# Optimization experiments

Hardware: AMD Instinct MI355X
Metric: run time of the kernel (lower is better)

## Reference

```python
import jax, jax.numpy as jnp
import numpy as np

NUM_HEADS = 16

def _rope(t, cos, sin):
    # t: [B,H,T,hd]; cos/sin: [T,half]
    half = t.shape[-1] // 2
    t1, t2 = t[..., :half], t[..., half:]
    return jnp.concatenate((t1 * cos - t2 * sin, t1 * sin + t2 * cos), axis=-1)

def setup_inputs() -> dict:
    key = jax.random.key(0)
    ks = jax.random.split(key, 5)
    B, T, D = 2, 2048, 2048
    s = 0.02
    return {
        'x': jax.random.normal(ks[0], (B, T, D), jnp.float32),
        'w_qkv': jax.random.normal(ks[1], (3 * D, D), jnp.float32) * s,
        'b_qkv': jax.random.normal(ks[2], (3 * D,), jnp.float32) * s,
        'w_out': jax.random.normal(ks[3], (D, D), jnp.float32) * s,
        'b_out': jax.random.normal(ks[4], (D,), jnp.float32) * s,
    }

def reference(x, w_qkv, b_qkv, w_out, b_out):
    B, T, D = x.shape
    H = NUM_HEADS
    hd = D // H
    half = hd // 2
    # fused QKV projection (torch Linear: x @ W^T + b)
    qkv = (x @ w_qkv.T + b_qkv).reshape(B, T, H, 3, hd)
    q, k, v = qkv[..., 0, :], qkv[..., 1, :], qkv[..., 2, :]
    q, k, v = (jnp.transpose(t, (0, 2, 1, 3)) for t in (q, k, v))  # [B,H,T,hd]
    # RoPE frequencies (buffer computed as in __init__)
    theta = 1.0 / (10000.0 ** (jnp.arange(half, dtype=jnp.float32) / half))
    freq = jnp.arange(T, dtype=jnp.float32)[:, None] * theta[None, :]  # [T,half]
    cos, sin = jnp.cos(freq), jnp.sin(freq)
    q = _rope(q, cos, sin)
    k = _rope(k, cos, sin)
    # causal attention; NOTE: source scales by embed_dim**-0.5
    scale = D ** (-0.5)
    scores = jnp.einsum('bhqd,bhkd->bhqk', q, k) * scale
    mask = jnp.triu(jnp.full((T, T), -1e9, dtype=scores.dtype), k=1)
    weights = jax.nn.softmax(scores + mask, axis=-1)
    attn = jnp.einsum('bhqk,bhkd->bhqd', weights, v)
    attn = jnp.transpose(attn, (0, 2, 1, 3)).reshape(B, T, D)
    return attn @ w_out.T + b_out
```

## Files before the change

kernel.cpp:

```cpp
#include <hip/hip_runtime.h>
#include <math.h>

#define NHEAD 16
#define TSEQ  2048
#define BATCH 2
#define DM    2048

typedef __attribute__((ext_vector_type(8))) short bf16x8;
typedef __attribute__((ext_vector_type(4))) float f32x4;

__device__ __forceinline__ short f2bf(float f) {
    unsigned u = __builtin_bit_cast(unsigned, f);
    u += 0x7fff + ((u >> 16) & 1);
    return (short)(u >> 16);
}
__device__ __forceinline__ float bf2f(short s) {
    unsigned u = ((unsigned)(unsigned short)s) << 16;
    return __builtin_bit_cast(float, u);
}
__device__ __forceinline__ void gload_lds16(const void* g, void* l) {
    __builtin_amdgcn_global_load_lds(
        (const __attribute__((address_space(1))) unsigned int*)g,
        (__attribute__((address_space(3))) unsigned int*)l, 16, 0, 0);
}

__global__ __launch_bounds__(256)
void cast_all(const float* __restrict__ x, short* __restrict__ xb,
              const float* __restrict__ wq, short* __restrict__ wqb,
              const float* __restrict__ wo, short* __restrict__ wob,
              float2* __restrict__ trig)
{
    int bid = blockIdx.x;
    if (bid >= 12288) {
        if (trig) {
            int idx = (bid - 12288) * 256 + threadIdx.x;
            int d = idx >> 11, t = idx & 2047;
            float trev = exp2f(-(float)d * (13.287712379549449f / 64.0f))
                         * 0.15915494309189535f;
            float ang = (float)t * trev;
            float fr = ang - floorf(ang);
            float sn, cs;
            __sincosf(fr * 6.283185307179586f, &sn, &cs);
            trig[idx] = make_float2(cs, sn);
        }
        return;
    }
    const float* src; short* dst; int lb;
    if (bid < 4096)       { src = x;  dst = xb;  lb = bid; }
    else if (bid < 10240) { src = wq; dst = wqb; lb = bid - 4096; }
    else                  { src = wo; dst = wob; lb = bid - 10240; }
    int i = (lb * 256 + threadIdx.x) * 8;
    float4 a = *(const float4*)(src + i);
    float4 b = *(const float4*)(src + i + 4);
    bf16x8 o;
    o[0]=f2bf(a.x); o[1]=f2bf(a.y); o[2]=f2bf(a.z); o[3]=f2bf(a.w);
    o[4]=f2bf(b.x); o[5]=f2bf(b.y); o[6]=f2bf(b.z); o[7]=f2bf(b.w);
    *(bf16x8*)(dst + i) = o;
}

#define BARRIER() __builtin_amdgcn_s_barrier()
#define WAIT_LGKM0() do { asm volatile("s_waitcnt lgkmcnt(0)" ::: "memory"); \
                          __builtin_amdgcn_sched_barrier(0); } while (0)
#define WAIT_VM(N) asm volatile("s_waitcnt vmcnt(" #N ")" ::: "memory")

#define LOAD_A(BUF, MH) do {                                                  \
    const short* base_ = sm + (BUF)*32768 + (MH)*8192;                        \
    _Pragma("unroll")                                                         \
    for (int m_ = 0; m_ < 4; ++m_) {                                          \
        int j_ = wr*64 + m_*16 + lane15;                                      \
        const short* rp_ = base_ + j_*64;                                     \
        int sw_ = (j_ & 7) << 3;                                              \
        af[m_][0] = *(const bf16x8*)(rp_ + ((quad << 3) ^ sw_));              \
        af[m_][1] = *(const bf16x8*)(rp_ + ((32 + (quad << 3)) ^ sw_));       \
    }                                                                         \
} while (0)

#define LOAD_B(BUF, NH, BB) do {                                              \
    const short* base_ = sm + (BUF)*32768 + 16384 + (NH)*8192;                \
    _Pragma("unroll")                                                         \
    for (int n_ = 0; n_ < 2; ++n_) {                                          \
        int j_ = wc*32 + n_*16 + lane15;                                      \
        const short* rp_ = base_ + j_*64;                                     \
        int sw_ = (j_ & 7) << 3;                                              \
        BB[n_][0] = *(const bf16x8*)(rp_ + ((quad << 3) ^ sw_));              \
        BB[n_][1] = *(const bf16x8*)(rp_ + ((32 + (quad << 3)) ^ sw_));       \
    }                                                                         \
} while (0)

#define STAGE_A(T, MH, BUFOFF) do { if ((T) < 32) {                           \
    short* dst_ = sm + (BUFOFF) + ((MH) << 13);                               \
    _Pragma("unroll")                                                         \
    for (int i_ = 0; i_ < 2; ++i_)                                            \
        gload_lds16(pAsrc[i_][MH] + ((T) << 6), dst_ + (i_*512 + tid)*8);     \
    } } while (0)

#define STAGE_B(T, NH, BUFOFF) do { if ((T) < 32) {                           \
    short* dst_ = sm + (BUFOFF) + 16384 + ((NH) << 13);                       \
    _Pragma("unroll")                                                         \
    for (int i_ = 0; i_ < 2; ++i_)                                            \
        gload_lds16(pWsrc[i_][NH] + ((T) << 6), dst_ + (i_*512 + tid)*8);     \
    } } while (0)

#define MMA_Q(MH, NH, BB) do {                                                \
    _Pragma("unroll")                                                         \
    for (int m_ = 0; m_ < 4; ++m_) {                                          \
        _Pragma("unroll")                                                     \
        for (int n_ = 0; n_ < 2; ++n_) {                                      \
            f32x4 c_ = acc[(MH)*4 + m_][(NH)*2 + n_];                         \
            c_ = __builtin_amdgcn_mfma_f32_16x16x32_bf16(af[m_][0], BB[n_][0], c_, 0, 0, 0); \
            c_ = __builtin_amdgcn_mfma_f32_16x16x32_bf16(af[m_][1], BB[n_][1], c_, 0, 0, 0); \
            acc[(MH)*4 + m_][(NH)*2 + n_] = c_;                               \
        }                                                                     \
    }                                                                         \
} while (0)

__global__ __launch_bounds__(512, 2)
void gemm_qkv_rope(const short* __restrict__ A, const short* __restrict__ W,
                   const float* __restrict__ bias, short* __restrict__ qfrag,
                   short* __restrict__ kfrag, short* __restrict__ vfrag,
                   const float2* __restrict__ trig)
{
    __shared__ short sm[65536];
    const int tid = threadIdx.x;
    const int lane = tid & 63, w = tid >> 6;
    const int lane15 = lane & 15, quad = lane >> 4;
    const int wr = w >> 2, wc = w & 3;
    const int row0 = blockIdx.y * 256, col0 = blockIdx.x * 256;

    const short* pAsrc[2][2];
    const short* pWsrc[2][2];
    #pragma unroll
    for (int i_ = 0; i_ < 2; ++i_) {
        int ci = i_*512 + tid, j = ci >> 3, lc = ci & 7;
        int swz = (lc ^ (j & 7)) << 3;
        #pragma unroll
        for (int h = 0; h < 2; ++h) {
            pAsrc[i_][h] = A + (size_t)(row0 + (j & 63) + ((j >> 6) << 7) + h*64) * 2048 + swz;
            pWsrc[i_][h] = W + (size_t)(col0 + (j & 31) + ((j >> 5) << 6) + h*32) * 2048 + swz;
        }
    }

    f32x4 acc[8][4];
    #pragma unroll
    for (int mi = 0; mi < 8; ++mi)
        #pragma unroll
        for (int ni = 0; ni < 4; ++ni)
            acc[mi][ni] = (f32x4){0.f, 0.f, 0.f, 0.f};

    bf16x8 af[4][2], bb0[2][2], bb1[2][2];

    STAGE_A(0, 0, 0);     STAGE_B(0, 0, 0);
    STAGE_A(0, 1, 0);     STAGE_B(0, 1, 0);
    STAGE_A(1, 0, 32768); STAGE_B(1, 0, 32768);
    STAGE_A(1, 1, 32768); STAGE_B(1, 1, 32768);
    WAIT_VM(8);
    BARRIER();

    for (int i = 0; i < 16; ++i) {
        const int ta = 2*i + 2;
        const int tb = 2*i + 3;
        LOAD_A(0, 0);
        LOAD_B(0, 0, bb0);
        BARRIER(); WAIT_LGKM0();
        __builtin_amdgcn_s_setprio(1); MMA_Q(0, 0, bb0); __builtin_amdgcn_s_setprio(0);
        BARRIER();
        LOAD_B(0, 1, bb1);
        STAGE_A(ta, 0, 0); STAGE_B(ta, 0, 0);
        BARRIER(); WAIT_LGKM0();
        __builtin_amdgcn_s_setprio(1); MMA_Q(0, 1, bb1); __builtin_amdgcn_s_setprio(0);
        BARRIER();
        LOAD_A(0, 1);
        STAGE_B(ta, 1, 0);
        BARRIER(); WAIT_LGKM0();
        __builtin_amdgcn_s_setprio(1); MMA_Q(1, 1, bb1); __builtin_amdgcn_s_setprio(0);
        BARRIER();
        STAGE_A(ta, 1, 0);
        if (i == 15) { WAIT_VM(0); } else { WAIT_VM(8); }
        BARRIER();
        __builtin_amdgcn_s_setprio(1); MMA_Q(1, 0, bb0); __builtin_amdgcn_s_setprio(0);
        BARRIER();
        LOAD_A(1, 0);
        LOAD_B(1, 0, bb0);
        BARRIER(); WAIT_LGKM0();
        __builtin_amdgcn_s_setprio(1); MMA_Q(0, 0, bb0); __builtin_amdgcn_s_setprio(0);
        BARRIER();
        LOAD_B(1, 1, bb1);
        STAGE_A(tb, 0, 32768); STAGE_B(tb, 0, 32768);
        BARRIER(); WAIT_LGKM0();
        __builtin_amdgcn_s_setprio(1); MMA_Q(0, 1, bb1); __builtin_amdgcn_s_setprio(0);
        BARRIER();
        LOAD_A(1, 1);
        STAGE_B(tb, 1, 32768);
        BARRIER(); WAIT_LGKM0();
        __builtin_amdgcn_s_setprio(1); MMA_Q(1, 1, bb1); __builtin_amdgcn_s_setprio(0);
        BARRIER();
        STAGE_A(tb, 1, 32768);
        if (i < 15) { WAIT_VM(8); }
        BARRIER();
        __builtin_amdgcn_s_setprio(1); MMA_Q(1, 0, bb0); __builtin_amdgcn_s_setprio(0);
        BARRIER();
    }

    const int b = row0 >> 11;
    const int t0g = row0 & 2047;
    #pragma unroll
    for (int ch = 0; ch < 2; ++ch) {
        const int cidx = (col0 >> 7) + ch;
        const int head = cidx / 3, type = cidx % 3;
        __syncthreads();
        if ((wc >> 1) == ch) {
            #pragma unroll
            for (int ni = 0; ni < 4; ++ni) {
                int d = (wc & 1)*64 + ni*16 + lane15;
                float bv = bias[col0 + ch*128 + d];
                #pragma unroll
                for (int mi = 0; mi < 8; ++mi) {
                    int rowb = wr*128 + mi*16 + quad*4;
                    #pragma unroll
                    for (int r = 0; r < 4; ++r)
                        sm[(rowb + r)*136 + d] = f2bf(acc[mi][ni][r] + bv);
                }
            }
        }
        __syncthreads();
        if (type < 2) {
            const float sc = (type == 0) ? 0.022097086912079608f : 1.0f;
            short* dst = (type == 0 ? qfrag : kfrag) + (size_t)(b*NHEAD + head)*262144;
            #pragma unroll
            for (int it = 0; it < 4; ++it) {
                int c = it*512 + tid;
                int l15 = c & 15, q_ = (c >> 4) & 3, kc = (c >> 6) & 1, rowhi = c >> 7;
                int lrow = rowhi*16 + l15;
                int t = t0g + lrow;
                bf16x8 a8 = *(const bf16x8*)(sm + lrow*136 + kc*32 + q_*8);
                bf16x8 b8 = *(const bf16x8*)(sm + lrow*136 + kc*32 + q_*8 + 64);
                bf16x8 oa, ob;
                if (trig) {
                    const float2* tg = trig + (size_t)(kc*32 + q_*8)*2048 + t;
                    #pragma unroll
                    for (int j = 0; j < 8; ++j) {
                        float2 cs2 = tg[(size_t)j*2048];
                        float va = bf2f(a8[j]), vb = bf2f(b8[j]);
                        oa[j] = f2bf((va*cs2.x - vb*cs2.y)*sc);
                        ob[j] = f2bf((va*cs2.y + vb*cs2.x)*sc);
                    }
                } else {
                    #pragma unroll
                    for (int j = 0; j < 8; ++j) {
                        int d = kc*32 + q_*8 + j;
                        float trev = exp2f(-(float)d * (13.287712379549449f / 64.0f))
                                     * 0.15915494309189535f;
                        float ang = (float)t * trev;
                        float fr = ang - floorf(ang);
                        float sn, cs;
                        __sincosf(fr * 6.283185307179586f, &sn, &cs);
                        float va = bf2f(a8[j]), vb = bf2f(b8[j]);
                        oa[j] = f2bf((va*cs - vb*sn)*sc);
                        ob[j] = f2bf((va*sn + vb*cs)*sc);
                    }
                }
                size_t base = (size_t)((t0g >> 4) + rowhi)*2048 + (q_*16 + l15)*8;
                *(bf16x8*)(dst + base + kc*512)        = oa;
                *(bf16x8*)(dst + base + kc*512 + 1024) = ob;
            }
        } else {
            short* dst = vfrag + (size_t)(b*NHEAD + head)*262144;
            #pragma unroll
            for (int it = 0; it < 8; ++it) {
                int c = it*512 + tid;
                int lane_ = c & 63, rest = c >> 6;
                int q_ = lane_ >> 4, l15 = lane_ & 15;
                int dt = rest & 7, kc2 = (rest >> 3) & 1, kbt = rest >> 4;
                int d = dt*16 + l15;
                bf16x8 v;
                #pragma unroll
                for (int j = 0; j < 8; ++j)
                    v[j] = sm[(kbt*64 + kc2*32 + q_*8 + j)*136 + d];
                *(bf16x8*)(dst + (size_t)((t0g >> 6) + kbt)*8192
                            + dt*1024 + kc2*512 + lane_*8) = v;
            }
        }
    }
}

__global__ __launch_bounds__(256)
void gemm_out(const short* __restrict__ A, const short* __restrict__ W,
              const float* __restrict__ bias, float* __restrict__ Cout,
              int N, int K)
{
    __shared__ short As[128 * 64];
    __shared__ short Bs[128 * 64];
    const int tid = threadIdx.x;
    const int lane = tid & 63, w = tid >> 6;
    const int lane15 = lane & 15, quad = lane >> 4;
    const int wr = w >> 1, wc = w & 1;
    const int row0 = blockIdx.y * 128, col0 = blockIdx.x * 128;

    f32x4 acc[4][4];
    #pragma unroll
    for (int mi = 0; mi < 4; ++mi)
        #pragma unroll
        for (int ni = 0; ni < 4; ++ni)
            acc[mi][ni] = (f32x4){0.f, 0.f, 0.f, 0.f};

    for (int kt = 0; kt < K; kt += 64) {
        __syncthreads();
        #pragma unroll
        for (int i = 0; i < 4; ++i) {
            int ci = i * 256 + tid;
            int row = ci >> 3, lc = ci & 7;
            int gc = lc ^ (row & 7);
            gload_lds16(A + (size_t)(row0 + row) * K + kt + gc * 8, As + ci * 8);
            gload_lds16(W + (size_t)(col0 + row) * K + kt + gc * 8, Bs + ci * 8);
        }
        __syncthreads();
        #pragma unroll
        for (int kc = 0; kc < 2; ++kc) {
            bf16x8 af[4], bfr[4];
            #pragma unroll
            for (int mi = 0; mi < 4; ++mi) {
                int r = wr * 64 + mi * 16 + lane15;
                af[mi] = *(const bf16x8*)(As + r * 64 + ((kc * 4 + quad) ^ (r & 7)) * 8);
            }
            #pragma unroll
            for (int ni = 0; ni < 4; ++ni) {
                int r = wc * 64 + ni * 16 + lane15;
                bfr[ni] = *(const bf16x8*)(Bs + r * 64 + ((kc * 4 + quad) ^ (r & 7)) * 8);
            }
            #pragma unroll
            for (int mi = 0; mi < 4; ++mi)
                #pragma unroll
                for (int ni = 0; ni < 4; ++ni)
                    acc[mi][ni] = __builtin_amdgcn_mfma_f32_16x16x32_bf16(
                        af[mi], bfr[ni], acc[mi][ni], 0, 0, 0);
        }
    }

    #pragma unroll
    for (int mi = 0; mi < 4; ++mi)
        #pragma unroll
        for (int ni = 0; ni < 4; ++ni) {
            int col = col0 + wc * 64 + ni * 16 + lane15;
            float bv = bias[col];
            #pragma unroll
            for (int r = 0; r < 4; ++r) {
                int row = row0 + wr * 64 + mi * 16 + quad * 4 + r;
                Cout[(size_t)row * N + col] = acc[mi][ni][r] + bv;
            }
        }
}

__global__ __launch_bounds__(256)
void attn3(const short* __restrict__ qfrag, const short* __restrict__ kfrag,
           const short* __restrict__ vfrag, short* __restrict__ attnb)
{
    __shared__ short KV[2][16384];
    __shared__ short Pb[4][1152];
    const int tid = threadIdx.x;
    const int lane = tid & 63, w = tid >> 6;
    const int lane15 = lane & 15, quad = lane >> 4;
    const int g = (blockIdx.x + blockIdx.y) & 15;
    const int qb = blockIdx.z ? (15 - g) : g;
    const int h = blockIdx.y, b = blockIdx.z;
    const int bh = b * NHEAD + h;
    const int q0 = qb * 128;
    short* Pw = Pb[w];

    bf16x8 qf[2][4];
    {
        const short* qp = qfrag + (size_t)bh * 262144
                        + (size_t)(qb * 8 + w * 2) * 2048 + lane * 8;
        #pragma unroll
        for (int nq = 0; nq < 2; ++nq)
            #pragma unroll
            for (int kc = 0; kc < 4; ++kc)
                qf[nq][kc] = *(const bf16x8*)(qp + nq * 2048 + kc * 512);
    }

    f32x4 acc[8][2];
    #pragma unroll
    for (int dt = 0; dt < 8; ++dt)
        #pragma unroll
        for (int nq = 0; nq < 2; ++nq)
            acc[dt][nq] = (f32x4){0.f, 0.f, 0.f, 0.f};
    float m_s[2] = {-3e38f, -3e38f}, l_s[2] = {0.f, 0.f};

    const short* kf_src = kfrag + (size_t)bh * 262144;
    const short* vf_src = vfrag + (size_t)bh * 262144;
    const int kb_max = 2 * qb + 1;
    const int qtop = q0 + w * 32 + 31;
    const int diag0 = (q0 + w * 32) >> 6;

    #pragma unroll
    for (int i = 0; i < 4; ++i) {
        int ci = i * 256 + tid;
        gload_lds16(kf_src + ci * 8, KV[0] + ci * 8);
        gload_lds16(vf_src + ci * 8, KV[0] + 8192 + ci * 8);
    }

    for (int kb = 0; kb <= kb_max; ++kb) {
        __syncthreads();
        if (kb < kb_max) {
            const short* ks = kf_src + (size_t)(kb + 1) * 8192;
            const short* vs = vf_src + (size_t)(kb + 1) * 8192;
            short* kd = KV[(kb + 1) & 1];
            #pragma unroll
            for (int i = 0; i < 4; ++i) {
                int ci = i * 256 + tid;
                gload_lds16(ks + ci * 8, kd + ci * 8);
                gload_lds16(vs + ci * 8, kd + 8192 + ci * 8);
            }
        }
        if (kb * 64 > qtop) continue;
        const short* Ks = KV[kb & 1];
        const short* Vs = Ks + 8192;

        f32x4 st[2][4];
        #pragma unroll
        for (int nq = 0; nq < 2; ++nq)
            #pragma unroll
            for (int mi = 0; mi < 4; ++mi)
                st[nq][mi] = (f32x4){0.f, 0.f, 0.f, 0.f};
        #pragma unroll
        for (int mi = 0; mi < 4; ++mi) {
            bf16x8 kf4[4];
            #pragma unroll
            for (int kc = 0; kc < 4; ++kc)
                kf4[kc] = *(const bf16x8*)(Ks + ((mi * 4 + kc) * 64 + lane) * 8);
            #pragma unroll
            for (int kc = 0; kc < 4; ++kc)
                #pragma unroll
                for (int nq = 0; nq < 2; ++nq)
                    st[nq][mi] = __builtin_amdgcn_mfma_f32_16x16x32_bf16(
                        kf4[kc], qf[nq][kc], st[nq][mi], 0, 0, 0);
        }

        if (kb >= diag0) {
            #pragma unroll
            for (int nq = 0; nq < 2; ++nq) {
                int qg = q0 + w * 32 + nq * 16 + lane15;
                #pragma unroll
                for (int mi = 0; mi < 4; ++mi)
                    #pragma unroll
                    for (int r = 0; r < 4; ++r)
                        if (kb * 64 + mi * 16 + quad * 4 + r > qg)
                            st[nq][mi][r] = -3e38f;
            }
        }

        bf16x8 pb[2][2];
        #pragma unroll
        for (int nq = 0; nq < 2; ++nq) {
            float mt = st[nq][0][0];
            #pragma unroll
            for (int mi = 0; mi < 4; ++mi)
                #pragma unroll
                for (int r = 0; r < 4; ++r)
                    mt = fmaxf(mt, st[nq][mi][r]);
            mt = fmaxf(mt, __shfl_xor(mt, 16));
            mt = fmaxf(mt, __shfl_xor(mt, 32));
            float mn = fmaxf(m_s[nq], mt);
            float alpha = __expf(m_s[nq] - mn);
            m_s[nq] = mn;
            float sum = 0.f;
            #pragma unroll
            for (int mi = 0; mi < 4; ++mi)
                #pragma unroll
                for (int r = 0; r < 4; ++r) {
                    float p = __expf(st[nq][mi][r] - mn);
                    st[nq][mi][r] = p;
                    sum += p;
                }
            sum += __shfl_xor(sum, 16);
            sum += __shfl_xor(sum, 32);
            l_s[nq] = l_s[nq] * alpha + sum;
            #pragma unroll
            for (int dt = 0; dt < 8; ++dt) {
                acc[dt][nq][0] *= alpha; acc[dt][nq][1] *= alpha;
                acc[dt][nq][2] *= alpha; acc[dt][nq][3] *= alpha;
            }
            short* pr = Pw + lane15 * 72 + quad * 4;
            #pragma unroll
            for (int mi = 0; mi < 4; ++mi) {
                unsigned lo = (unsigned)(unsigned short)f2bf(st[nq][mi][0])
                            | ((unsigned)(unsigned short)f2bf(st[nq][mi][1]) << 16);
                unsigned hi = (unsigned)(unsigned short)f2bf(st[nq][mi][2])
                            | ((unsigned)(unsigned short)f2bf(st[nq][mi][3]) << 16);
                *(unsigned*)(pr + mi * 16)     = lo;
                *(unsigned*)(pr + mi * 16 + 2) = hi;
            }
            __asm__ volatile("s_waitcnt lgkmcnt(0)" ::: "memory");
            #pragma unroll
            for (int kc2 = 0; kc2 < 2; ++kc2)
                pb[nq][kc2] = *(const bf16x8*)(Pw + lane15 * 72 + kc2 * 32 + quad * 8);
            __asm__ volatile("s_waitcnt lgkmcnt(0)" ::: "memory");
        }

        #pragma unroll
        for (int dt = 0; dt < 8; ++dt)
            #pragma unroll
            for (int kc2 = 0; kc2 < 2; ++kc2) {
                bf16x8 vf = *(const bf16x8*)(Vs + ((dt * 2 + kc2) * 64 + lane) * 8);
                #pragma unroll
                for (int nq = 0; nq < 2; ++nq)
                    acc[dt][nq] = __builtin_amdgcn_mfma_f32_16x16x32_bf16(
                        vf, pb[nq][kc2], acc[dt][nq], 0, 0, 0);
            }
    }

    __syncthreads();
    short* Eb = KV[0];
    #pragma unroll
    for (int nq = 0; nq < 2; ++nq) {
        float inv = 1.f / l_s[nq];
        int qrow = w * 32 + nq * 16 + lane15;
        #pragma unroll
        for (int dt = 0; dt < 8; ++dt) {
            unsigned lo = (unsigned)(unsigned short)f2bf(acc[dt][nq][0] * inv)
                        | ((unsigned)(unsigned short)f2bf(acc[dt][nq][1] * inv) << 16);
            unsigned hi = (unsigned)(unsigned short)f2bf(acc[dt][nq][2] * inv)
                        | ((unsigned)(unsigned short)f2bf(acc[dt][nq][3] * inv) << 16);
            *(unsigned*)(Eb + qrow * 136 + dt * 16 + quad * 4)     = lo;
            *(unsigned*)(Eb + qrow * 136 + dt * 16 + quad * 4 + 2) = hi;
        }
    }
    __syncthreads();
    {
        int r = tid >> 1, half = tid & 1;
        short* orow = attnb + (size_t)(b * TSEQ + q0 + r) * DM + h * 128 + half * 64;
        #pragma unroll
        for (int i = 0; i < 8; ++i)
            *(bf16x8*)(orow + i * 8) =
                *(const bf16x8*)(Eb + r * 136 + half * 64 + i * 8);
    }
}

extern "C" void kernel_launch(void* const* d_in, const int* in_sizes, int n_in,
                              void* d_out, int out_size, void* d_ws, size_t ws_size,
                              hipStream_t stream)
{
    const float* x     = (const float*)d_in[0];
    const float* w_qkv = (const float*)d_in[1];
    const float* b_qkv = (const float*)d_in[2];
    const float* w_out = (const float*)d_in[3];
    const float* b_out = (const float*)d_in[4];
    float* out = (float*)d_out;

    char* ws = (char*)d_ws;
    short* xb    = (short*)(ws);
    short* wqkvb = (short*)(ws + 16777216);
    short* woutb = (short*)(ws + 41943040);
    short* qfrag = (short*)(ws + 50331648);
    short* kfrag = (short*)(ws + 67108864);
    short* vfrag = (short*)(ws + 83886080);
    short* attnb = xb;
    float2* trig = (ws_size >= 100663296ull + 1048576ull)
                 ? (float2*)(ws + 100663296) : nullptr;

    {
        int grid = trig ? 12800 : 12288;
        cast_all<<<grid, 256, 0, stream>>>(x, xb, w_qkv, wqkvb, w_out, woutb, trig);
    }
    {
        dim3 g2(24, 16);
        gemm_qkv_rope<<<g2, 512, 0, stream>>>(xb, wqkvb, b_qkv, qfrag, kfrag, vfrag, trig);
    }
    {
        dim3 g2(16, NHEAD, BATCH);
        attn3<<<g2, 256, 0, stream>>>(qfrag, kfrag, vfrag, attnb);
    }
    {
        dim3 g2(16, 32);
        gemm_out<<<g2, 256, 0, stream>>>(attnb, woutb, b_out, out, 2048, 2048);
    }
}
```

Before: 380.8 us.

## Pipeline output GEMM with triple-buffered LDS and 128x256 tiles

Rewrites the output projection GEMM to use 512 threads per block computing 128x256 tiles. Global-to-LDS loads for two stages ahead go into a three-slot ring buffer, with vmcnt waits and setprio around the MFMA bursts. This overlaps memory loads with matrix math and halves the W reloads per output, at the cost of more LDS (144KB) and only 256 blocks, which risks lower occupancy and tail imbalance.

Result: no change. 388.2 us (+1.9%).

```diff
diff --git a/kernel.cpp b/kernel.cpp
--- a/kernel.cpp
+++ b/kernel.cpp
@@ -283,18 +283,56 @@
     }
 }
 
-__global__ __launch_bounds__(256)
+#define OSTAGE(T) do { if ((T) < 32) {                                        \
+    short* dst_ = smo + ((T) % 3) * 24576;                                    \
+    const int kt_ = (T) << 6;                                                 \
+    _Pragma("unroll")                                                         \
+    for (int i_ = 0; i_ < 2; ++i_) {                                          \
+        int ci_ = i_*512 + tid;                                               \
+        int r_ = ci_ >> 3, lc_ = ci_ & 7;                                     \
+        gload_lds16(A + (size_t)(row0 + r_)*2048 + kt_ + ((lc_ ^ (r_ & 7)) << 3), \
+                    dst_ + ci_*8);                                            \
+    }                                                                         \
+    _Pragma("unroll")                                                         \
+    for (int i_ = 0; i_ < 4; ++i_) {                                          \
+        int ci_ = i_*512 + tid;                                               \
+        int r_ = ci_ >> 3, lc_ = ci_ & 7;                                     \
+        gload_lds16(W + (size_t)(col0 + r_)*2048 + kt_ + ((lc_ ^ (r_ & 7)) << 3), \
+                    dst_ + 8192 + ci_*8);                                     \
+    } } } while (0)
+
+#define OLRD(Ab, Bb, KC) do {                                                 \
+    _Pragma("unroll")                                                         \
+    for (int m_ = 0; m_ < 4; ++m_) {                                          \
+        int r_ = wr*64 + m_*16 + lane15;                                      \
+        af[m_] = *(const bf16x8*)((Ab) + r_*64 + ((((KC)*4 + quad) ^ (r_ & 7)) << 3)); \
+    }                                                                         \
+    _Pragma("unroll")                                                         \
+    for (int n_ = 0; n_ < 4; ++n_) {                                          \
+        int r_ = wc*64 + n_*16 + lane15;                                      \
+        bb[n_] = *(const bf16x8*)((Bb) + r_*64 + ((((KC)*4 + quad) ^ (r_ & 7)) << 3)); \
+    }                                                                         \
+} while (0)
+
+#define OMMA() do {                                                           \
+    _Pragma("unroll")                                                         \
+    for (int m_ = 0; m_ < 4; ++m_)                                            \
+        _Pragma("unroll")                                                     \
+        for (int n_ = 0; n_ < 4; ++n_)                                        \
+            acc[m_][n_] = __builtin_amdgcn_mfma_f32_16x16x32_bf16(            \
+                af[m_], bb[n_], acc[m_][n_], 0, 0, 0);                        \
+} while (0)
+
+__global__ __launch_bounds__(512, 2)
 void gemm_out(const short* __restrict__ A, const short* __restrict__ W,
-              const float* __restrict__ bias, float* __restrict__ Cout,
-              int N, int K)
+              const float* __restrict__ bias, float* __restrict__ Cout)
 {
-    __shared__ short As[128 * 64];
-    __shared__ short Bs[128 * 64];
+    __shared__ short smo[73728];
     const int tid = threadIdx.x;
     const int lane = tid & 63, w = tid >> 6;
     const int lane15 = lane & 15, quad = lane >> 4;
-    const int wr = w >> 1, wc = w & 1;
-    const int row0 = blockIdx.y * 128, col0 = blockIdx.x * 128;
+    const int wr = w >> 2, wc = w & 3;
+    const int row0 = blockIdx.y * 128, col0 = blockIdx.x * 256;
 
     f32x4 acc[4][4];
     #pragma unroll
@@ -303,49 +341,37 @@
         for (int ni = 0; ni < 4; ++ni)
             acc[mi][ni] = (f32x4){0.f, 0.f, 0.f, 0.f};
 
-    for (int kt = 0; kt < K; kt += 64) {
-        __syncthreads();
-        #pragma unroll
-        for (int i = 0; i < 4; ++i) {
-            int ci = i * 256 + tid;
-            int row = ci >> 3, lc = ci & 7;
-            int gc = lc ^ (row & 7);
-            gload_lds16(A + (size_t)(row0 + row) * K + kt + gc * 8, As + ci * 8);
-            gload_lds16(W + (size_t)(col0 + row) * K + kt + gc * 8, Bs + ci * 8);
-        }
-        __syncthreads();
-        #pragma unroll
-        for (int kc = 0; kc < 2; ++kc) {
-            bf16x8 af[4], bfr[4];
-            #pragma unroll
-            for (int mi = 0; mi < 4; ++mi) {
-                int r = wr * 64 + mi * 16 + lane15;
-                af[mi] = *(const bf16x8*)(As + r * 64 + ((kc * 4 + quad) ^ (r & 7)) * 8);
-            }
-            #pragma unroll
-            for (int ni = 0; ni < 4; ++ni) {
-                int r = wc * 64 + ni * 16 + lane15;
-                bfr[ni] = *(const bf16x8*)(Bs + r * 64 + ((kc * 4 + quad) ^ (r & 7)) * 8);
-            }
-            #pragma unroll
-            for (int mi = 0; mi < 4; ++mi)
-                #pragma unroll
-                for (int ni = 0; ni < 4; ++ni)
-                    acc[mi][ni] = __builtin_amdgcn_mfma_f32_16x16x32_bf16(
-                        af[mi], bfr[ni], acc[mi][ni], 0, 0, 0);
-        }
+    bf16x8 af[4], bb[4];
+
+    OSTAGE(0); OSTAGE(1);
+    WAIT_VM(6);
+    BARRIER();
+
+    for (int t = 0; t < 32; ++t) {
+        short* Ab = smo + (t % 3) * 24576;
+        short* Bb = Ab + 8192;
+        OLRD(Ab, Bb, 0);
+        OSTAGE(t + 2);
+        BARRIER(); WAIT_LGKM0();
+        __builtin_amdgcn_s_setprio(1); OMMA(); __builtin_amdgcn_s_setprio(0);
+        BARRIER();
+        OLRD(Ab, Bb, 1);
+        if (t < 30) { WAIT_VM(6); } else { WAIT_VM(0); }
+        BARRIER(); WAIT_LGKM0();
+        __builtin_amdgcn_s_setprio(1); OMMA(); __builtin_amdgcn_s_setprio(0);
+        BARRIER();
     }
 
     #pragma unroll
     for (int mi = 0; mi < 4; ++mi)
         #pragma unroll
         for (int ni = 0; ni < 4; ++ni) {
-            int col = col0 + wc * 64 + ni * 16 + lane15;
+            int col = col0 + wc*64 + ni*16 + lane15;
             float bv = bias[col];
             #pragma unroll
             for (int r = 0; r < 4; ++r) {
-                int row = row0 + wr * 64 + mi * 16 + quad * 4 + r;
-                Cout[(size_t)row * N + col] = acc[mi][ni][r] + bv;
+                int row = row0 + wr*64 + mi*16 + quad*4 + r;
+                Cout[(size_t)row*2048 + col] = acc[mi][ni][r] + bv;
             }
         }
 }
@@ -570,7 +596,7 @@
         attn3<<<g2, 256, 0, stream>>>(qfrag, kfrag, vfrag, attnb);
     }
     {
-        dim3 g2(16, 32);
-        gemm_out<<<g2, 256, 0, stream>>>(attnb, woutb, b_out, out, 2048, 2048);
-    }
-}
+        dim3 g2(8, 32);
+        gemm_out<<<g2, 512, 0, stream>>>(attnb, woutb, b_out, out);
+    }
+}
```
